# Optimization experiments

Hardware: AMD Instinct MI355X
Metric: run time of the kernel (lower is better)

Reference implementation:

```python
import jax, jax.numpy as jnp
import numpy as np

N_NODES = 20000
N_EDGES = 640000
N_TRIP = 1000000
C = 128          # channels
E = 64           # expansion_features
CUTOFF = 5.0
LOG2 = float(np.log(2.0))


def ssp(x):
    # ShiftedSoftplus
    return jax.nn.softplus(x) - LOG2


def setup_inputs() -> dict:
    key = jax.random.key(0)
    ks = jax.random.split(key, 12)
    features = jax.random.normal(ks[0], (N_NODES, C), dtype=jnp.float32)
    neighbour_distances = jax.random.uniform(ks[1], (N_EDGES,), dtype=jnp.float32) * (1.2 * CUTOFF)
    neighbour_list = jax.random.randint(ks[2], (2, N_EDGES), 0, N_NODES, dtype=jnp.int32)
    triplet_idxs = jax.random.randint(ks[3], (N_TRIP, 3), 0, N_NODES, dtype=jnp.int32)
    angles = jax.random.uniform(ks[4], (N_TRIP,), dtype=jnp.float32) * np.pi
    r_ij = jax.random.uniform(ks[5], (N_TRIP,), dtype=jnp.float32) * CUTOFF
    r_ik = jax.random.uniform(ks[6], (N_TRIP,), dtype=jnp.float32) * CUTOFF
    # learned parameters (Linear layers without bias; stored [in, out])
    W_pre = jax.random.normal(ks[7], (C, C), dtype=jnp.float32) / np.sqrt(C)
    W2b1 = jax.random.normal(ks[8], (E, E), dtype=jnp.float32) / np.sqrt(E)
    W2b2 = jax.random.normal(ks[9], (E, C), dtype=jnp.float32) / np.sqrt(E)
    W3b1 = jax.random.normal(ks[10], (3, C // 2), dtype=jnp.float32) / np.sqrt(3.0)
    W3b2 = jax.random.normal(ks[11], (C // 2, C), dtype=jnp.float32) / np.sqrt(C // 2)
    W_post = jax.random.normal(jax.random.fold_in(key, 99), (C, C), dtype=jnp.float32) / np.sqrt(C)
    return {
        "features": features,
        "neighbour_distances": neighbour_distances,
        "neighbour_list": neighbour_list,
        "triplet_idxs": triplet_idxs,
        "angles": angles,
        "r_ij": r_ij,
        "r_ik": r_ik,
        "W_pre": W_pre,
        "W2b1": W2b1,
        "W2b2": W2b2,
        "W3b1": W3b1,
        "W3b2": W3b2,
        "W_post": W_post,
    }


def reference(features, neighbour_distances, neighbour_list, triplet_idxs,
              angles, r_ij, r_ik, W_pre, W2b1, W2b2, W3b1, W3b2, W_post):
    # 1) pre-linear
    h = features @ W_pre                                   # [N, C]

    # 2) radial basis (Gaussian smearing) with smooth cosine cutoff envelope
    centers = jnp.linspace(0.0, CUTOFF, E, dtype=jnp.float32)  # [E]
    width = CUTOFF / E
    gamma = 1.0 / (2.0 * width * width)
    d = neighbour_distances[:, None]                       # [n_edges, 1]
    rb = jnp.exp(-gamma * (d - centers) ** 2)              # [n_edges, E]
    cutoff_mask = (neighbour_distances < CUTOFF).astype(jnp.float32)
    cutoff_values = 0.5 * (1.0 + jnp.cos(np.pi * neighbour_distances / CUTOFF))
    rb = rb * (cutoff_values * cutoff_mask)[:, None]       # fused envelope

    # 3) two-body messages: gather neighbour node features, modulate by radial MLP
    neighbor_h = h[neighbour_list[1]]                      # [n_edges, C]
    two_body = neighbor_h * (ssp(rb @ W2b1) @ W2b2)        # [n_edges, C]

    # 4) three-body messages: angular MLP on (r_ij, r_ik, cos(angle)),
    #    gather node features at triplet_idxs[:,1], scatter-add into edge slots
    tbf = jnp.stack([r_ij, r_ik, jnp.cos(angles)], axis=-1)  # [n_trip, 3]
    w3 = ssp(tbf @ W3b1) @ W3b2                              # [n_trip, C]
    msgs = h[triplet_idxs[:, 1]] * w3                        # [n_trip, C]
    edge_msgs = jnp.zeros_like(two_body).at[triplet_idxs[:, 1]].add(msgs)

    # 5) aggregate messages over neighbours (to central atom = neighbour_list[0])
    messages = two_body + edge_msgs
    agg = jax.ops.segment_sum(messages, neighbour_list[0], num_segments=N_NODES)

    # 6) post-linear
    return agg @ W_post
```

## Files before the change

### kernel.cpp

```cpp
#include <hip/hip_runtime.h>
#include <hip/hip_fp16.h>
#include <math.h>

#define TID threadIdx.x

typedef ushort u16x8 __attribute__((ext_vector_type(8)));
typedef unsigned char uchar;

static constexpr int NN = 20000;
static constexpr int NE = 640000;
static constexpr int NT = 1000000;
static constexpr int C = 128;
static constexpr int E = 64;
static constexpr int LUTN = 4104;
static constexpr int NBKT = 313;
static constexpr int NB2 = 512;
static constexpr int CHE2 = 1250;
static constexpr int CHT2 = 1954;
static constexpr float CUT = 5.0f;
static constexpr float LN2 = 0.69314718055994530942f;

__device__ __forceinline__ float ssp(float x) {
    return fmaxf(x, 0.0f) + __logf(1.0f + __expf(-fabsf(x))) - LN2;
}

__device__ __forceinline__ ushort f2bf(float x) {
    uint u = __float_as_uint(x);
    return (ushort)((u + 0x7FFFu + ((u >> 16) & 1u)) >> 16);
}

__device__ __forceinline__ float bf2f(ushort u) {
    return __uint_as_float((uint)u << 16);
}

__device__ __forceinline__ float h2f(uint bits) {
    return __half2float(__ushort_as_half((ushort)(bits & 0xFFFFu)));
}

__global__ __launch_bounds__(256) void k_gemm16f(const float* __restrict__ A,
                                                 const float* __restrict__ W,
                                                 float* __restrict__ out, int nrows) {
    __shared__ ushort wB[C * C];
    __shared__ float aL[16][132];
    for (int i = TID; i < C * C / 4; i += 256) {
        float4 w4 = ((const float4*)W)[i];
        ushort4 u = {f2bf(w4.x), f2bf(w4.y), f2bf(w4.z), f2bf(w4.w)};
        ((ushort4*)wB)[i] = u;
    }
    const int base = blockIdx.x * 16;
    for (int i = TID; i < 512; i += 256) {
        int r = base + (i >> 5);
        float4 v = (r < nrows) ? ((const float4*)A)[(size_t)r * 32 + (i & 31)]
                               : (float4){0.f, 0.f, 0.f, 0.f};
        *(float4*)&aL[i >> 5][(i & 31) << 2] = v;
    }
    __syncthreads();
    const int rg = TID >> 4;
    const int c8 = (TID & 15) << 3;
    float acc[8] = {0.f, 0.f, 0.f, 0.f, 0.f, 0.f, 0.f, 0.f};
    #pragma unroll 8
    for (int k = 0; k < C; ++k) {
        float a = aL[rg][k];
        u16x8 wv = *(const u16x8*)&wB[k * C + c8];
        #pragma unroll
        for (int j = 0; j < 8; ++j) acc[j] = fmaf(a, bf2f(wv[j]), acc[j]);
    }
    int r = base + rg;
    if (r < nrows) {
        float4 o0 = {acc[0], acc[1], acc[2], acc[3]};
        float4 o1 = {acc[4], acc[5], acc[6], acc[7]};
        *(float4*)&out[(size_t)r * C + c8] = o0;
        *(float4*)&out[(size_t)r * C + c8 + 4] = o1;
    }
}

__global__ __launch_bounds__(256) void k_gemm16b(const float* __restrict__ A,
                                                 const float* __restrict__ W,
                                                 ushort* __restrict__ outB, int nrows) {
    __shared__ ushort wB[C * C];
    __shared__ float aL[16][132];
    for (int i = TID; i < C * C / 4; i += 256) {
        float4 w4 = ((const float4*)W)[i];
        ushort4 u = {f2bf(w4.x), f2bf(w4.y), f2bf(w4.z), f2bf(w4.w)};
        ((ushort4*)wB)[i] = u;
    }
    const int base = blockIdx.x * 16;
    for (int i = TID; i < 512; i += 256) {
        int r = base + (i >> 5);
        float4 v = (r < nrows) ? ((const float4*)A)[(size_t)r * 32 + (i & 31)]
                               : (float4){0.f, 0.f, 0.f, 0.f};
        *(float4*)&aL[i >> 5][(i & 31) << 2] = v;
    }
    __syncthreads();
    const int rg = TID >> 4;
    const int c8 = (TID & 15) << 3;
    float acc[8] = {0.f, 0.f, 0.f, 0.f, 0.f, 0.f, 0.f, 0.f};
    #pragma unroll 8
    for (int k = 0; k < C; ++k) {
        float a = aL[rg][k];
        u16x8 wv = *(const u16x8*)&wB[k * C + c8];
        #pragma unroll
        for (int j = 0; j < 8; ++j) acc[j] = fmaf(a, bf2f(wv[j]), acc[j]);
    }
    int r = base + rg;
    if (r < nrows) {
        u16x8 u;
        #pragma unroll
        for (int j = 0; j < 8; ++j) u[j] = f2bf(acc[j]);
        *(u16x8*)&outB[(size_t)r * C + c8] = u;
    }
}

__global__ __launch_bounds__(256) void k_lut(const float* __restrict__ W2b1,
                                             const float* __restrict__ W2b2,
                                             ushort* __restrict__ lutB,
                                             float2* __restrict__ spLut) {
    if (blockIdx.x == (LUTN + 7) / 8) {
        for (int e = TID; e < 512; e += 256) {
            float t0 = (float)e * (1.0f / 32.0f);
            float t1 = (float)(e + 1) * (1.0f / 32.0f);
            float v0 = log1pf(__expf(-t0));
            float v1 = log1pf(__expf(-t1));
            spLut[e] = make_float2(v0, v1 - v0);
        }
        return;
    }
    __shared__ float w1[E * E];
    __shared__ float w2[E * C];
    __shared__ float rbL[8][E];
    __shared__ float hid[8][E];
    for (int i = TID; i < E * E; i += 256) w1[i] = W2b1[i];
    for (int i = TID; i < E * C; i += 256) w2[i] = W2b2[i];
    const int jj = TID & 63;
    const int esA = TID >> 6;
    const int eg = TID >> 5;
    const int c4 = (TID & 31) << 2;
    const float gamma = 81.92f;
    const float cstep = CUT / 63.0f;
    const float delta = CUT / 4096.0f;
    const int base = blockIdx.x * 8;
    __syncthreads();
    #pragma unroll
    for (int s = 0; s < 2; ++s) {
        int es = esA + 4 * s;
        float d = (float)(base + es) * delta;
        float cv = (d < CUT) ? 0.5f * (1.0f + __cosf((float)M_PI * d / CUT)) : 0.0f;
        float dd = d - (float)jj * cstep;
        rbL[es][jj] = __expf(-gamma * dd * dd) * cv;
    }
    __syncthreads();
    #pragma unroll
    for (int s = 0; s < 2; ++s) {
        int es = esA + 4 * s;
        float a = 0.f;
        #pragma unroll 16
        for (int k = 0; k < E; ++k)
            a = fmaf(rbL[es][k], w1[k * E + jj], a);
        hid[es][jj] = ssp(a);
    }
    __syncthreads();
    float4 o = {0.f, 0.f, 0.f, 0.f};
    #pragma unroll
    for (int j = 0; j < E; ++j) {
        float t = hid[eg][j];
        const float4 w4 = *(const float4*)&w2[j * C + c4];
        o.x = fmaf(t, w4.x, o.x);
        o.y = fmaf(t, w4.y, o.y);
        o.z = fmaf(t, w4.z, o.z);
        o.w = fmaf(t, w4.w, o.w);
    }
    int row = base + eg;
    if (row < LUTN) {
        ushort4 u = {f2bf(o.x), f2bf(o.y), f2bf(o.z), f2bf(o.w)};
        *(ushort4*)&lutB[(size_t)row * C + c4] = u;
    }
}

__global__ __launch_bounds__(256) void k_bcount(const int* __restrict__ nl0,
                                                const int* __restrict__ tidx,
                                                uchar* __restrict__ cntE,
                                                uchar* __restrict__ cntT) {
    __shared__ int h[NBKT];
    const int b = blockIdx.x;
    for (int i = TID; i < NBKT; i += 256) h[i] = 0;
    __syncthreads();
    const int e0 = b * CHE2, e1 = min(e0 + CHE2, NE);
    for (int i = e0 + TID; i < e1; i += 256) atomicAdd(&h[nl0[i] >> 6], 1);
    __syncthreads();
    for (int i = TID; i < NBKT; i += 256) { cntE[(size_t)i * NB2 + b] = (uchar)h[i]; h[i] = 0; }
    __syncthreads();
    const int t0 = b * CHT2, t1 = min(t0 + CHT2, NT);
    for (int i = t0 + TID; i < t1; i += 256) atomicAdd(&h[tidx[3 * i + 1] >> 6], 1);
    __syncthreads();
    for (int i = TID; i < NBKT; i += 256) cntT[(size_t)i * NB2 + b] = (uchar)h[i];
}

__global__ __launch_bounds__(256) void k_bscan(const uchar* __restrict__ cE,
                                               const uchar* __restrict__ cT,
                                               ushort* __restrict__ baseE,
                                               ushort* __restrict__ baseT,
                                               int* __restrict__ totEb,
                                               int* __restrict__ totTb) {
    const int lane = TID & 63;
    const int wv = TID >> 6;
    int task = blockIdx.x * 4 + wv;
    if (task >= 2 * NBKT) return;
    const bool isE = task < NBKT;
    const int k = isE ? task : task - NBKT;
    const uchar* src = isE ? cE : cT;
    ushort* dst = isE ? baseE : baseT;
    int* dT = isE ? totEb : totTb;
    int v[8], pre[8], s = 0;
    #pragma unroll
    for (int j = 0; j < 8; ++j) {
        v[j] = src[(size_t)k * NB2 + lane * 8 + j];
        pre[j] = s;
        s += v[j];
    }
    int incl = s;
    #pragma unroll
    for (int off = 1; off < 64; off <<= 1) {
        int t = __shfl_up(incl, off, 64);
        if (lane >= off) incl += t;
    }
    int excl = incl - s;
    #pragma unroll
    for (int j = 0; j < 8; ++j)
        dst[(size_t)k * NB2 + lane * 8 + j] = (ushort)(excl + pre[j]);
    if (lane == 63) dT[k] = incl;
}

__device__ void scan_one(const int* __restrict__ hist, int* __restrict__ start, int n) {
    __shared__ int wsum[16];
    __shared__ int carryS;
    const int lane = TID & 63;
    const int wv = TID >> 6;
    if (TID == 0) carryS = 0;
    __syncthreads();
    for (int base = 0; base < n; base += 1024) {
        int i = base + TID;
        int v = (i < n) ? hist[i] : 0;
        int acc = v;
        #pragma unroll
        for (int off = 1; off < 64; off <<= 1) {
            int t = __shfl_up(acc, off, 64);
            if (lane >= off) acc += t;
        }
        if (lane == 63) wsum[wv] = acc;
        __syncthreads();
        int woff = 0;
        for (int w = 0; w < wv; ++w) woff += wsum[w];
        int excl = carryS + woff + acc - v;
        if (i < n) start[i] = excl;
        __syncthreads();
        if (TID == 1023) carryS = excl + v;
        __syncthreads();
    }
}

__global__ __launch_bounds__(1024) void k_bktscan(const int* __restrict__ totEb, int* __restrict__ bksE,
                                                  const int* __restrict__ totTb, int* __restrict__ bksT) {
    if (blockIdx.x == 0) scan_one(totEb, bksE, NBKT);
    else                 scan_one(totTb, bksT, NBKT);
}

__global__ __launch_bounds__(256) void k_bplace(const int* __restrict__ nl0,
                                                const int* __restrict__ nl1,
                                                const float* __restrict__ dist,
                                                const int* __restrict__ tidx,
                                                const float* __restrict__ angles,
                                                const float* __restrict__ rij,
                                                const float* __restrict__ rik,
                                                const ushort* __restrict__ baseE,
                                                const ushort* __restrict__ baseT,
                                                const int* __restrict__ bksE,
                                                const int* __restrict__ bksT,
                                                int2* __restrict__ eT,
                                                int2* __restrict__ tT) {
    __shared__ int cur[NBKT];
    const int b = blockIdx.x;
    for (int k = TID; k < NBKT; k += 256)
        cur[k] = bksE[k] + (int)baseE[(size_t)k * NB2 + b];
    __syncthreads();
    const int e0 = b * CHE2, e1 = min(e0 + CHE2, NE);
    for (int i = e0 + TID; i < e1; i += 256) {
        int n0 = nl0[i];
        int pos = atomicAdd(&cur[n0 >> 6], 1);
        uint tq = (uint)fmaf(dist[i], 209715.2f, 0.5f);
        eT[pos] = make_int2((int)(tq | ((uint)(n0 & 63) << 26)), nl1[i]);
    }
    __syncthreads();
    for (int k = TID; k < NBKT; k += 256)
        cur[k] = bksT[k] + (int)baseT[(size_t)k * NB2 + b];
    __syncthreads();
    const int t0 = b * CHT2, tEnd = min(t0 + CHT2, NT);
    for (int i = t0 + TID; i < tEnd; i += 256) {
        int t1 = tidx[3 * i + 1];
        int pos = atomicAdd(&cur[t1 >> 6], 1);
        uint ab = ((uint)__half_as_ushort(__float2half_rn(rik[i])) << 16)
                | (uint)__half_as_ushort(__float2half_rn(rij[i]));
        uint cc = (uint)__half_as_ushort(__float2half_rn(__cosf(angles[i])))
                | ((uint)(t1 & 63) << 16);
        tT[pos] = make_int2((int)ab, (int)cc);
    }
}

__global__ __launch_bounds__(256) void k_nsort(const int2* __restrict__ eTs,
                                               const int2* __restrict__ tTs,
                                               const int* __restrict__ bksE,
                                               const int* __restrict__ bksT,
                                               const int* __restrict__ totEb,
                                               const int* __restrict__ totTb,
                                               int2* __restrict__ eS,
                                               int2* __restrict__ tS,
                                               int* __restrict__ startE,
                                               int* __restrict__ totE,
                                               int* __restrict__ startT,
                                               int* __restrict__ totT) {
    __shared__ int hist[64];
    __shared__ int cur[64];
    const bool isE = blockIdx.x < NBKT;
    const int bkt = isE ? blockIdx.x : blockIdx.x - NBKT;
    const int2* src = isE ? eTs : tTs;
    int2* dst = isE ? eS : tS;
    const int s0 = isE ? bksE[bkt] : bksT[bkt];
    const int cnt = isE ? totEb[bkt] : totTb[bkt];
    int* stX = isE ? startE : startT;
    int* ttX = isE ? totE : totT;
    if (TID < 64) hist[TID] = 0;
    __syncthreads();
    for (int i = TID; i < cnt; i += 256) {
        int2 p = src[s0 + i];
        int nlo = isE ? (int)(((uint)p.x >> 26) & 63u) : (int)(((uint)p.y >> 16) & 63u);
        atomicAdd(&hist[nlo], 1);
    }
    __syncthreads();
    if (TID < 64) {
        int v = hist[TID];
        int incl = v;
        #pragma unroll
        for (int off = 1; off < 64; off <<= 1) {
            int t = __shfl_up(incl, off, 64);
            if (TID >= off) incl += t;
        }
        int excl = incl - v;
        cur[TID] = s0 + excl;
        int node = bkt * 64 + TID;
        if (node < NN) { stX[node] = s0 + excl; ttX[node] = v; }
    }
    __syncthreads();
    for (int i = TID; i < cnt; i += 256) {
        int2 p = src[s0 + i];
        int nlo = isE ? (int)(((uint)p.x >> 26) & 63u) : (int)(((uint)p.y >> 16) & 63u);
        int pos = atomicAdd(&cur[nlo], 1);
        dst[pos] = p;
    }
}

__global__ __launch_bounds__(256) void k_edges_node(const int2* __restrict__ eS,
                                                    const int* __restrict__ startE,
                                                    const int* __restrict__ totE,
                                                    const ushort* __restrict__ hB,
                                                    const ushort* __restrict__ lutB,
                                                    float* __restrict__ agg) {
    __shared__ int4 stage[4][2][64];
    const int lane = TID & 63;
    const int wv = TID >> 6;
    const int c2b = lane << 2;
    for (int r = blockIdx.x * 4 + wv; r < NN; r += gridDim.x * 4) {
        const int s0 = startE[r];
        const int cnt = totE[r];
        float a0 = 0.f, a1 = 0.f;
        int2 pf;
        if (lane < min(64, cnt)) pf = eS[s0 + lane];
        const int nch = (cnt + 63) >> 6;
        for (int c = 0; c < nch; ++c) {
            const int base = c << 6;
            const int n = min(64, cnt - base);
            const int slot = c & 1;
            if (lane < n) {
                uint tq = ((uint)pf.x) & 0x03FFFFFFu;
                int idx = min((int)(tq >> 8), LUTN - 2);
                float fr = (float)(tq & 255u) * (1.0f / 256.0f);
                stage[wv][slot][lane] = make_int4(idx * (C * 2), __float_as_int(fr),
                                                  pf.y * (C * 2), 0);
            }
            int nb = base + 64;
            if (nb < cnt && lane < cnt - nb) pf = eS[s0 + nb + lane];
            asm volatile("s_waitcnt lgkmcnt(0)" ::: "memory");
            #pragma unroll 8
            for (int i = 0; i < n; ++i) {
                int4 q = stage[wv][slot][i];
                float fr = __int_as_float(q.y);
                ushort2 A2 = *(const ushort2*)((const char*)lutB + q.x + c2b);
                ushort2 B2 = *(const ushort2*)((const char*)lutB + q.x + 256 + c2b);
                ushort2 H2 = *(const ushort2*)((const char*)hB + q.z + c2b);
                float ax = bf2f(A2.x), ay = bf2f(A2.y);
                float ox = fmaf(fr, bf2f(B2.x) - ax, ax);
                float oy = fmaf(fr, bf2f(B2.y) - ay, ay);
                a0 = fmaf(ox, bf2f(H2.x), a0);
                a1 = fmaf(oy, bf2f(H2.y), a1);
            }
        }
        asm volatile("s_waitcnt lgkmcnt(0)" ::: "memory");
        float2 o = {a0, a1};
        *(float2*)&agg[(size_t)r * C + (lane << 1)] = o;
    }
}

__global__ __launch_bounds__(256) void k_trip_node(const int* __restrict__ startT,
                                                   const int* __restrict__ totT,
                                                   const int2* __restrict__ tS,
                                                   const float* __restrict__ W3b1,
                                                   const float* __restrict__ W3b2,
                                                   const float2* __restrict__ spLut,
                                                   const ushort* __restrict__ hB,
                                                   const int* __restrict__ nl0,
                                                   float* __restrict__ agg) {
    __shared__ uint w2p[64 * 64];
    __shared__ uint spl[512];
    __shared__ float4 stage[4][2][64];
    for (int i = TID; i < 512; i += 256) {
        float2 vs = spLut[i];
        spl[i] = ((uint)f2bf(vs.y) << 16) | (uint)f2bf(vs.x);
    }
    for (int i = TID; i < 4096; i += 256) {
        int k = i >> 6, l = i & 63;
        w2p[i] = ((uint)f2bf(W3b2[k * C + 64 + l]) << 16) | (uint)f2bf(W3b2[k * C + l]);
    }
    __syncthreads();
    const int lane = TID & 63;
    const int wv = TID >> 6;
    const float w1a = W3b1[lane];
    const float w1b = W3b1[64 + lane];
    const float w1c = W3b1[128 + lane];
    for (int r = blockIdx.x * 4 + wv; r < NN; r += gridDim.x * 4) {
        const int s0 = startT[r];
        const int cnt = totT[r];
        float usA = 0.f, usB = 0.f;
        uint2 pf;
        if (lane < min(64, cnt)) pf = ((const uint2*)tS)[s0 + lane];
        const int nch = (cnt + 63) >> 6;
        for (int c = 0; c < nch; ++c) {
            const int base = c << 6;
            const int n = min(64, cnt - base);
            const int slot = c & 1;
            if (lane < n) {
                float4 f;
                f.x = h2f(pf.x);
                f.y = h2f(pf.x >> 16);
                f.z = h2f(pf.y);
                f.w = 0.f;
                stage[wv][slot][lane] = f;
            }
            int nb = base + 64;
            if (nb < cnt && lane < cnt - nb) pf = ((const uint2*)tS)[s0 + nb + lane];
            asm volatile("s_waitcnt lgkmcnt(0)" ::: "memory");
            int i = 0;
            #pragma unroll 4
            for (; i + 1 < n; i += 2) {
                float4 pa = stage[wv][slot][i];
                float4 pb = stage[wv][slot][i + 1];
                float xa = fmaf(pa.x, w1a, fmaf(pa.y, w1b, pa.z * w1c));
                float xb = fmaf(pb.x, w1a, fmaf(pb.y, w1b, pb.z * w1c));
                float ta = fabsf(xa) * 32.0f;
                float tb = fabsf(xb) * 32.0f;
                int ia = min((int)ta, 511);
                int ib = min((int)tb, 511);
                float fa = ta - (float)ia;
                float fb = tb - (float)ib;
                uint va = spl[ia];
                uint vb = spl[ib];
                usA += fmaxf(xa, 0.f) + fmaf(fa, bf2f((ushort)(va >> 16)), bf2f((ushort)va));
                usB += fmaxf(xb, 0.f) + fmaf(fb, bf2f((ushort)(vb >> 16)), bf2f((ushort)vb));
            }
            if (i < n) {
                float4 pa = stage[wv][slot][i];
                float xa = fmaf(pa.x, w1a, fmaf(pa.y, w1b, pa.z * w1c));
                float ta = fabsf(xa) * 32.0f;
                int ia = min((int)ta, 511);
                float fa = ta - (float)ia;
                uint va = spl[ia];
                usA += fmaxf(xa, 0.f) + fmaf(fa, bf2f((ushort)(va >> 16)), bf2f((ushort)va));
            }
        }
        asm volatile("s_waitcnt lgkmcnt(0)" ::: "memory");
        float usum = usA + usB - LN2 * (float)cnt;
        float o0 = 0.f, o1 = 0.f;
        #pragma unroll 8
        for (int k = 0; k < 64; ++k) {
            float uk = __shfl(usum, k, 64);
            uint wp = w2p[k * 64 + lane];
            o0 = fmaf(uk, __uint_as_float(wp << 16), o0);
            o1 = fmaf(uk, __uint_as_float(wp & 0xFFFF0000u), o1);
        }
        const int n0 = nl0[r];
        float h0 = bf2f(hB[(size_t)r * C + lane]);
        float h1 = bf2f(hB[(size_t)r * C + 64 + lane]);
        unsafeAtomicAdd(&agg[(size_t)n0 * C + lane], o0 * h0);
        unsafeAtomicAdd(&agg[(size_t)n0 * C + 64 + lane], o1 * h1);
    }
}

extern "C" void kernel_launch(void* const* d_in, const int* in_sizes, int n_in,
                              void* d_out, int out_size, void* d_ws, size_t ws_size,
                              hipStream_t stream) {
    const float* features = (const float*)d_in[0];
    const float* ndist    = (const float*)d_in[1];
    const int*   nlist    = (const int*)d_in[2];
    const int*   tidx     = (const int*)d_in[3];
    const float* angles   = (const float*)d_in[4];
    const float* rij      = (const float*)d_in[5];
    const float* rik      = (const float*)d_in[6];
    const float* W_pre    = (const float*)d_in[7];
    const float* W2b1     = (const float*)d_in[8];
    const float* W2b2     = (const float*)d_in[9];
    const float* W3b1     = (const float*)d_in[10];
    const float* W3b2     = (const float*)d_in[11];
    const float* W_post   = (const float*)d_in[12];
    float* out = (float*)d_out;

    char* w = (char*)d_ws;
    float* agg    = (float*)w;
    int2* eT      = (int2*)w;
    w += (size_t)NN * C * 4;
    ushort* hB    = (ushort*)w;  w += (size_t)NN * C * 2;
    ushort* lutB  = (ushort*)w;  w += (size_t)LUTN * C * 2;
    int2* eS      = (int2*)w;    w += (size_t)NE * 8;
    int2* tS      = (int2*)w;    w += (size_t)NT * 8;
    int2* tT      = (int2*)w;    w += (size_t)NT * 8;
    uchar* cntE   = (uchar*)w;   w += (size_t)NBKT * NB2;
    uchar* cntT   = (uchar*)w;   w += (size_t)NBKT * NB2;
    ushort* baseE = (ushort*)w;  w += (size_t)NBKT * NB2 * 2;
    ushort* baseT = (ushort*)w;  w += (size_t)NBKT * NB2 * 2;
    int* totEb    = (int*)w;     w += 1280;
    int* totTb    = (int*)w;     w += 1280;
    int* bksE     = (int*)w;     w += 1280;
    int* bksT     = (int*)w;     w += 1280;
    int* startE   = (int*)w;     w += (size_t)NN * 4;
    int* totE     = (int*)w;     w += (size_t)NN * 4;
    int* startT   = (int*)w;     w += (size_t)NN * 4;
    int* totT     = (int*)w;     w += (size_t)NN * 4;
    float2* spLut = (float2*)w;  w += 512 * 8;

    const int* nl0 = nlist;
    const int* nl1 = nlist + NE;

    hipLaunchKernelGGL(k_gemm16b, dim3((NN + 15) / 16), dim3(256), 0, stream,
                       features, W_pre, hB, NN);
    hipLaunchKernelGGL(k_lut, dim3((LUTN + 7) / 8 + 1), dim3(256), 0, stream,
                       W2b1, W2b2, lutB, spLut);
    hipLaunchKernelGGL(k_bcount, dim3(NB2), dim3(256), 0, stream,
                       nl0, tidx, cntE, cntT);
    hipLaunchKernelGGL(k_bscan, dim3((2 * NBKT + 3) / 4), dim3(256), 0, stream,
                       cntE, cntT, baseE, baseT, totEb, totTb);
    hipLaunchKernelGGL(k_bktscan, dim3(2), dim3(1024), 0, stream,
                       totEb, bksE, totTb, bksT);
    hipLaunchKernelGGL(k_bplace, dim3(NB2), dim3(256), 0, stream,
                       nl0, nl1, ndist, tidx, angles, rij, rik,
                       baseE, baseT, bksE, bksT, eT, tT);
    hipLaunchKernelGGL(k_nsort, dim3(2 * NBKT), dim3(256), 0, stream,
                       eT, tT, bksE, bksT, totEb, totTb,
                       eS, tS, startE, totE, startT, totT);
    hipLaunchKernelGGL(k_edges_node, dim3(2048), dim3(256), 0, stream,
                       eS, startE, totE, hB, lutB, agg);
    hipLaunchKernelGGL(k_trip_node, dim3(1536), dim3(256), 0, stream,
                       startT, totT, tS, W3b1, W3b2, spLut, hB, nl0, agg);
    hipLaunchKernelGGL(k_gemm16f, dim3((NN + 15) / 16), dim3(256), 0, stream,
                       agg, W_post, out, NN);
}
```

Baseline: 193.4 us.

## Split triplet node kernel: write hidden sums, apply W3b2 in separate tiled kernel

The triplet kernel now only accumulates the per-node 64-wide softplus hidden sums and stores them to a workspace buffer (aliased over the tT scratch). It no longer stages W3b2 in shared memory, does the shuffle-based matvec, or issues atomics. A new k_node_final kernel does the 64x128 projection on tiles of 16 nodes using bf16 weights in shared memory and 8-wide vector loads, then multiplies by h and atomically adds into agg. This cuts per-wave LDS setup and shuffle cost and lowers the triplet kernel's shared-memory footprint, which may raise occupancy. The cost is an extra launch plus a round trip of the intermediate through global memory, and the triplet kernel now runs before the edge kernel with a larger grid.

```diff
diff --git a/kernel.cpp b/kernel.cpp
--- a/kernel.cpp
+++ b/kernel.cpp
@@ -412,21 +412,13 @@
                                                    const int* __restrict__ totT,
                                                    const int2* __restrict__ tS,
                                                    const float* __restrict__ W3b1,
-                                                   const float* __restrict__ W3b2,
                                                    const float2* __restrict__ spLut,
-                                                   const ushort* __restrict__ hB,
-                                                   const int* __restrict__ nl0,
-                                                   float* __restrict__ agg) {
-    __shared__ uint w2p[64 * 64];
+                                                   float* __restrict__ uacc) {
     __shared__ uint spl[512];
     __shared__ float4 stage[4][2][64];
     for (int i = TID; i < 512; i += 256) {
         float2 vs = spLut[i];
         spl[i] = ((uint)f2bf(vs.y) << 16) | (uint)f2bf(vs.x);
-    }
-    for (int i = TID; i < 4096; i += 256) {
-        int k = i >> 6, l = i & 63;
-        w2p[i] = ((uint)f2bf(W3b2[k * C + 64 + l]) << 16) | (uint)f2bf(W3b2[k * C + l]);
     }
     __syncthreads();
     const int lane = TID & 63;
@@ -485,21 +477,47 @@
             }
         }
         asm volatile("s_waitcnt lgkmcnt(0)" ::: "memory");
-        float usum = usA + usB - LN2 * (float)cnt;
-        float o0 = 0.f, o1 = 0.f;
-        #pragma unroll 8
-        for (int k = 0; k < 64; ++k) {
-            float uk = __shfl(usum, k, 64);
-            uint wp = w2p[k * 64 + lane];
-            o0 = fmaf(uk, __uint_as_float(wp << 16), o0);
-            o1 = fmaf(uk, __uint_as_float(wp & 0xFFFF0000u), o1);
-        }
-        const int n0 = nl0[r];
-        float h0 = bf2f(hB[(size_t)r * C + lane]);
-        float h1 = bf2f(hB[(size_t)r * C + 64 + lane]);
-        unsafeAtomicAdd(&agg[(size_t)n0 * C + lane], o0 * h0);
-        unsafeAtomicAdd(&agg[(size_t)n0 * C + 64 + lane], o1 * h1);
-    }
+        uacc[(size_t)r * 64 + lane] = usA + usB - LN2 * (float)cnt;
+    }
+}
+
+__global__ __launch_bounds__(256) void k_node_final(const float* __restrict__ uacc,
+                                                    const float* __restrict__ W3b2,
+                                                    const ushort* __restrict__ hB,
+                                                    const int* __restrict__ nl0,
+                                                    float* __restrict__ agg) {
+    __shared__ ushort w2[64 * C];
+    __shared__ float uL[16][68];
+    for (int i = TID; i < 64 * C / 4; i += 256) {
+        float4 w4 = ((const float4*)W3b2)[i];
+        ushort4 u = {f2bf(w4.x), f2bf(w4.y), f2bf(w4.z), f2bf(w4.w)};
+        ((ushort4*)w2)[i] = u;
+    }
+    const int base = blockIdx.x * 16;
+    {
+        int i = TID;
+        int row = i >> 4, col = (i & 15) << 2;
+        float4 v = ((const float4*)uacc)[(size_t)(base + row) * 16 + (i & 15)];
+        *(float4*)&uL[row][col] = v;
+    }
+    __syncthreads();
+    const int rg = TID >> 4;
+    const int c8 = (TID & 15) << 3;
+    float acc[8] = {0.f, 0.f, 0.f, 0.f, 0.f, 0.f, 0.f, 0.f};
+    #pragma unroll 8
+    for (int k = 0; k < 64; ++k) {
+        float a = uL[rg][k];
+        u16x8 wv = *(const u16x8*)&w2[k * C + c8];
+        #pragma unroll
+        for (int j = 0; j < 8; ++j) acc[j] = fmaf(a, bf2f(wv[j]), acc[j]);
+    }
+    const int r = base + rg;
+    const int n0 = nl0[r];
+    u16x8 hv = *(const u16x8*)&hB[(size_t)r * C + c8];
+    float* dst = &agg[(size_t)n0 * C + c8];
+    #pragma unroll
+    for (int j = 0; j < 8; ++j)
+        unsafeAtomicAdd(dst + j, acc[j] * bf2f(hv[j]));
 }
 
 extern "C" void kernel_launch(void* const* d_in, const int* in_sizes, int n_in,
@@ -528,7 +546,9 @@
     ushort* lutB  = (ushort*)w;  w += (size_t)LUTN * C * 2;
     int2* eS      = (int2*)w;    w += (size_t)NE * 8;
     int2* tS      = (int2*)w;    w += (size_t)NT * 8;
-    int2* tT      = (int2*)w;    w += (size_t)NT * 8;
+    int2* tT      = (int2*)w;
+    float* uacc   = (float*)w;
+    w += (size_t)NT * 8;
     uchar* cntE   = (uchar*)w;   w += (size_t)NBKT * NB2;
     uchar* cntT   = (uchar*)w;   w += (size_t)NBKT * NB2;
     ushort* baseE = (ushort*)w;  w += (size_t)NBKT * NB2 * 2;
@@ -562,10 +582,12 @@
     hipLaunchKernelGGL(k_nsort, dim3(2 * NBKT), dim3(256), 0, stream,
                        eT, tT, bksE, bksT, totEb, totTb,
                        eS, tS, startE, totE, startT, totT);
+    hipLaunchKernelGGL(k_trip_node, dim3(2048), dim3(256), 0, stream,
+                       startT, totT, tS, W3b1, spLut, uacc);
     hipLaunchKernelGGL(k_edges_node, dim3(2048), dim3(256), 0, stream,
                        eS, startE, totE, hB, lutB, agg);
-    hipLaunchKernelGGL(k_trip_node, dim3(1536), dim3(256), 0, stream,
-                       startT, totT, tS, W3b1, W3b2, spLut, hB, nl0, agg);
+    hipLaunchKernelGGL(k_node_final, dim3(NN / 16), dim3(256), 0, stream,
+                       uacc, W3b2, hB, nl0, agg);
     hipLaunchKernelGGL(k_gemm16f, dim3((NN + 15) / 16), dim3(256), 0, stream,
                        agg, W_post, out, NN);
 }
```

New measurement: 250.0 us. +29.3%, slower.
